# Optimization experiments

Measured on AMD Instinct MI355X. Metric: run time of the kernel, lower is better.

## Reference

```python
import jax, jax.numpy as jnp
import numpy as np

H = 16       # num_attention_heads
HKV = 4      # num_key_value_heads
D = 128      # head_dim
CHUNK = 64   # input_chunk_size
RBS = 64     # retrieval_block_size


def setup_inputs() -> dict:
    key = jax.random.key(0)
    ks = jax.random.split(key, 9)
    B, S, HID = 1, 2048, 2048
    RLEN = 2048  # retrieval_block_num * RBS = (S // CHUNK) * RBS
    inv = 0.02
    return {
        "hidden_states": jax.random.normal(ks[0], (B, S, HID), jnp.float32),
        "cos": jax.random.uniform(ks[1], (B, S, D), jnp.float32),
        "sin": jax.random.uniform(ks[2], (B, S, D), jnp.float32),
        "retrieval_k": jax.random.normal(ks[3], (B, HKV, RLEN, D), jnp.float32),
        "retrieval_v": jax.random.normal(ks[4], (B, HKV, RLEN, D), jnp.float32),
        "Wq": jax.random.normal(ks[5], (HID, H * D), jnp.float32) * inv,
        "Wk": jax.random.normal(ks[6], (HID, HKV * D), jnp.float32) * inv,
        "Wv": jax.random.normal(ks[7], (HID, HKV * D), jnp.float32) * inv,
        "Wo": jax.random.normal(ks[8], (H * D, HID), jnp.float32) * inv,
    }


def _rope(x, cos, sin):
    # x: [B, h, S, D]; cos/sin: [B, S, D] (HF apply_rotary_pos_emb, unsqueeze head dim)
    c = cos[:, None, :, :]
    s = sin[:, None, :, :]
    x1, x2 = jnp.split(x, 2, axis=-1)
    rot = jnp.concatenate([-x2, x1], axis=-1)
    return x * c + rot * s


def reference(hidden_states, cos, sin, retrieval_k, retrieval_v, Wq, Wk, Wv, Wo):
    B, S, HID = hidden_states.shape
    G = H // HKV
    scale = D ** -0.5

    q = (hidden_states @ Wq).reshape(B, S, H, D).transpose(0, 2, 1, 3)    # [B,H,S,D]
    k = (hidden_states @ Wk).reshape(B, S, HKV, D).transpose(0, 2, 1, 3)  # [B,HKV,S,D]
    v = (hidden_states @ Wv).reshape(B, S, HKV, D).transpose(0, 2, 1, 3)

    q = _rope(q, cos, sin)
    k = _rope(k, cos, sin)

    # GQA: expand kv heads
    k_full = jnp.repeat(k, G, axis=1)  # [B,H,S,D]
    v_full = jnp.repeat(v, G, axis=1)

    # ---- causal part over input keys ----
    s1 = jnp.einsum('bhqd,bhkd->bhqk', q, k_full) * scale
    causal = jnp.tril(jnp.ones((S, S), bool))
    s1 = jnp.where(causal[None, None], s1, -jnp.inf)

    # ---- retrieval part: chunk c attends retrieval block (c-1) only ----
    C = S // CHUNK
    R = retrieval_k.shape[2] // RBS
    rK = retrieval_k.reshape(B, HKV, R, RBS, D)
    rV = retrieval_v.reshape(B, HKV, R, RBS, D)
    blk_idx = jnp.clip(jnp.arange(C) - 1, 0, R - 1)          # chunk 0 masked below
    rK_sel = jnp.repeat(rK[:, :, blk_idx], G, axis=1)        # [B,H,C,RBS,D]
    rV_sel = jnp.repeat(rV[:, :, blk_idx], G, axis=1)
    qc = q.reshape(B, H, C, CHUNK, D)
    s2 = jnp.einsum('bhcqd,bhckd->bhcqk', qc, rK_sel) * scale
    valid = (jnp.arange(C) >= 1)[None, None, :, None, None]
    s2 = jnp.where(valid, s2, -jnp.inf)

    # ---- joint (numerically stable) softmax over causal + retrieval keys ----
    m1 = jnp.max(s1, axis=-1)                                # [B,H,S]
    m2 = jnp.max(s2, axis=-1).reshape(B, H, S)               # -inf for chunk 0
    m = jnp.maximum(m1, m2)
    e1 = jnp.exp(s1 - m[..., None])
    e2 = jnp.exp(s2 - m.reshape(B, H, C, CHUNK)[..., None])
    denom = e1.sum(-1) + e2.sum(-1).reshape(B, H, S)         # [B,H,S]
    o1 = jnp.einsum('bhqk,bhkd->bhqd', e1, v_full)
    o2 = jnp.einsum('bhcqk,bhckd->bhcqd', e2, rV_sel).reshape(B, H, S, D)
    attn = (o1 + o2) / denom[..., None]                      # [B,H,S,D]

    out = attn.transpose(0, 2, 1, 3).reshape(B, S, H * D)
    return out @ Wo
```

## Files before the change

### kernel.cpp

```cpp
#include <hip/hip_runtime.h>
#include <stdint.h>

#define H_    16
#define HKV_  4
#define D_    128
#define S_    2048
#define HID_  2048
#define RLEN_ 2048

typedef unsigned short u16;
typedef __attribute__((ext_vector_type(4))) float f32x4;
typedef __attribute__((ext_vector_type(16))) float f32x16;
typedef __attribute__((ext_vector_type(8))) __bf16 bf16x8;
typedef __attribute__((ext_vector_type(4))) unsigned short u16x4;
typedef __attribute__((ext_vector_type(8))) unsigned short u16x8;
typedef __attribute__((ext_vector_type(2))) unsigned int u32x2;

__device__ __forceinline__ u16 f2bf(float f) {
  union { float f; unsigned u; } v; v.f = f;
  unsigned r = v.u + 0x7FFFu + ((v.u >> 16) & 1u);
  return (u16)(r >> 16);
}
__device__ __forceinline__ float bf2f(u16 h) {
  union { unsigned u; float f; } v; v.u = ((unsigned)h) << 16;
  return v.f;
}
__device__ __forceinline__ float lo2f(unsigned w) {
  union { unsigned u; float f; } v; v.u = w << 16; return v.f;
}
__device__ __forceinline__ float hi2f(unsigned w) {
  union { unsigned u; float f; } v; v.u = w & 0xFFFF0000u; return v.f;
}
__device__ __forceinline__ float exp2v(float x) {
  float r; asm("v_exp_f32 %0, %1" : "=v"(r) : "v"(x)); return r;
}
__device__ __forceinline__ unsigned cvtpk(float lo, float hi) {
  unsigned r; asm("v_cvt_pk_bf16_f32 %0, %1, %2" : "=v"(r) : "v"(lo), "v"(hi)); return r;
}
__device__ __forceinline__ void pl32swap(unsigned &a, unsigned &b) {
  u32x2 r = __builtin_amdgcn_permlane32_swap(a, b, false, false);
  a = r.x; b = r.y;
}
__device__ __forceinline__ float xhalf_max(float v) {
  unsigned a = __float_as_uint(v), b = a;
  pl32swap(a, b);
  return fmaxf(__uint_as_float(a), __uint_as_float(b));
}
__device__ __forceinline__ float xhalf_add(float v) {
  unsigned a = __float_as_uint(v), b = a;
  pl32swap(a, b);
  return __uint_as_float(a) + __uint_as_float(b);
}
__device__ __forceinline__ void drain_then_sync() {
  asm volatile("s_waitcnt vmcnt(0) lgkmcnt(0)" ::: "memory");
  __syncthreads();
}

#define GLL(srcp, ldsp) \
  __builtin_amdgcn_global_load_lds((const __attribute__((address_space(1))) unsigned int*)(srcp), \
                                   (__attribute__((address_space(3))) unsigned int*)(ldsp), 16, 0, 0)

__global__ void k_cvt(const float* __restrict__ in, u16* __restrict__ out, int n4) {
  int i = blockIdx.x * 256 + threadIdx.x;
  if (i >= n4) return;
  float4 v = ((const float4*)in)[i];
  u16x4 o;
  o.x = f2bf(v.x); o.y = f2bf(v.y); o.z = f2bf(v.z); o.w = f2bf(v.w);
  ((u16x4*)out)[i] = o;
}

__global__ void k_transw_qkv(const float* __restrict__ Wq, const float* __restrict__ Wk,
                             const float* __restrict__ Wv, u16* __restrict__ wtq) {
  __shared__ float tile[32][33];
  const int bid = blockIdx.x;
  const float* in; u16* out; int N, bx, by;
  if (bid < 4096)      { in = Wq; out = wtq;                          N = 2048; bx = (bid & 63) * 32;        by = (bid >> 6) * 32; }
  else if (bid < 5120) { in = Wk; out = wtq + (size_t)2048 * 2048;    N = 512;  bx = ((bid - 4096) & 15) * 32; by = ((bid - 4096) >> 4) * 32; }
  else                 { in = Wv; out = wtq + (size_t)2560 * 2048;    N = 512;  bx = ((bid - 5120) & 15) * 32; by = ((bid - 5120) >> 4) * 32; }
  const int K = 2048;
  int tx = threadIdx.x, ty = threadIdx.y;
#pragma unroll
  for (int i = 0; i < 32; i += 8)
    tile[ty + i][tx] = in[(size_t)(by + ty + i) * N + bx + tx];
  __syncthreads();
#pragma unroll
  for (int i = 0; i < 32; i += 8)
    out[(size_t)(bx + ty + i) * K + by + tx] = f2bf(tile[tx][ty + i]);
}

__global__ void k_transw(const float* __restrict__ in, u16* __restrict__ out, int K, int N) {
  __shared__ float tile[32][33];
  int bx = blockIdx.x * 32, by = blockIdx.y * 32;
  int tx = threadIdx.x, ty = threadIdx.y;
#pragma unroll
  for (int i = 0; i < 32; i += 8)
    tile[ty + i][tx] = in[(size_t)(by + ty + i) * N + bx + tx];
  __syncthreads();
#pragma unroll
  for (int i = 0; i < 32; i += 8)
    out[(size_t)(bx + ty + i) * K + by + tx] = f2bf(tile[tx][ty + i]);
}

__global__ __launch_bounds__(256) void k_gemm(const u16* __restrict__ A, const u16* __restrict__ Bt,
                                              u16* __restrict__ Cb, int M, int N, int K,
                                              int Kpart, int Krem) {
  __shared__ __attribute__((aligned(16))) u16 As[2][128 * 32];
  __shared__ __attribute__((aligned(16))) u16 Bs[2][128 * 32];
  const int bm = blockIdx.y * 128, bn = blockIdx.x * 128;
  const int kz0 = blockIdx.z * Kpart;
  const int kz1 = kz0 + Kpart + ((blockIdx.z == gridDim.z - 1) ? Krem : 0);
  u16* C = Cb + (size_t)blockIdx.z * M * N;
  const int tid = threadIdx.x, wave = tid >> 6, lane = tid & 63;
  const int wr = wave >> 1, wc = wave & 1;
  const int l15 = lane & 15, lhi = lane >> 4;
  const int so = wave * 512;
  f32x4 acc[4][4] = {};
  const u16* pA  = A  + (size_t)(bm + (tid >> 2)) * K + (tid & 3) * 8;
  const u16* pA2 = A  + (size_t)(bm + 64 + (tid >> 2)) * K + (tid & 3) * 8;
  const u16* pB  = Bt + (size_t)(bn + (tid >> 2)) * K + (tid & 3) * 8;
  const u16* pB2 = Bt + (size_t)(bn + 64 + (tid >> 2)) * K + (tid & 3) * 8;

  GLL(pA + kz0,  &As[0][so]);
  GLL(pA2 + kz0, &As[0][2048 + so]);
  GLL(pB + kz0,  &Bs[0][so]);
  GLL(pB2 + kz0, &Bs[0][2048 + so]);
  drain_then_sync();

  int buf = 0;
  for (int k0 = kz0; k0 < kz1; k0 += 32) {
    const int nb = buf ^ 1;
    if (k0 + 32 < kz1) {
      GLL(pA + k0 + 32,  &As[nb][so]);
      GLL(pA2 + k0 + 32, &As[nb][2048 + so]);
      GLL(pB + k0 + 32,  &Bs[nb][so]);
      GLL(pB2 + k0 + 32, &Bs[nb][2048 + so]);
    }
    bf16x8 af[4], bfr[4];
#pragma unroll
    for (int m = 0; m < 4; m++)
      af[m] = *(const bf16x8*)(&As[buf][(wr * 64 + m * 16 + l15) * 32 + lhi * 8]);
#pragma unroll
    for (int n = 0; n < 4; n++)
      bfr[n] = *(const bf16x8*)(&Bs[buf][(wc * 64 + n * 16 + l15) * 32 + lhi * 8]);
#pragma unroll
    for (int m = 0; m < 4; m++)
#pragma unroll
      for (int n = 0; n < 4; n++)
        acc[m][n] = __builtin_amdgcn_mfma_f32_16x16x32_bf16(af[m], bfr[n], acc[m][n], 0, 0, 0);
    drain_then_sync();
    buf = nb;
  }
  const int r0 = bm + wr * 64, c0 = bn + wc * 64;
#pragma unroll
  for (int m = 0; m < 4; m++)
#pragma unroll
    for (int n = 0; n < 4; n++) {
      int r = r0 + m * 16 + lhi * 4, cc = c0 + n * 16 + l15;
#pragma unroll
      for (int j = 0; j < 4; j++)
        C[(size_t)(r + j) * N + cc] = f2bf(acc[m][n][j]);
    }
}

__global__ void k_comb2(const u16* __restrict__ c0, const u16* __restrict__ c1,
                        float* __restrict__ out, int n8) {
  int i = blockIdx.x * 256 + threadIdx.x;
  if (i >= n8) return;
  u16x8 a = ((const u16x8*)c0)[i];
  u16x8 b = ((const u16x8*)c1)[i];
  float4 o0, o1;
  o0.x = bf2f(a[0]) + bf2f(b[0]); o0.y = bf2f(a[1]) + bf2f(b[1]);
  o0.z = bf2f(a[2]) + bf2f(b[2]); o0.w = bf2f(a[3]) + bf2f(b[3]);
  o1.x = bf2f(a[4]) + bf2f(b[4]); o1.y = bf2f(a[5]) + bf2f(b[5]);
  o1.z = bf2f(a[6]) + bf2f(b[6]); o1.w = bf2f(a[7]) + bf2f(b[7]);
  ((float4*)out)[i * 2]     = o0;
  ((float4*)out)[i * 2 + 1] = o1;
}

__global__ void k_ropeq(const u16* __restrict__ qp0, const float* __restrict__ cs,
                        const float* __restrict__ sn, u16* __restrict__ Q) {
  const u16* qp1 = qp0 + (size_t)2048 * 3072;
  int tid = threadIdx.x;
  int idx = blockIdx.x * 4 + (tid >> 6);
  int d = tid & 63;
  int h = idx >> 11, s = idx & (S_ - 1);
  size_t base = (size_t)s * 3072 + h * 128;
  float x1 = bf2f(qp0[base + d])      + bf2f(qp1[base + d]);
  float x2 = bf2f(qp0[base + d + 64]) + bf2f(qp1[base + d + 64]);
  float c1 = cs[s * D_ + d], s1v = sn[s * D_ + d];
  float c2 = cs[s * D_ + d + 64], s2v = sn[s * D_ + d + 64];
  const float sc = 0.12751744422f;
  u16* o = Q + ((size_t)h * S_ + s) * D_;
  o[d]      = f2bf((x1 * c1 - x2 * s1v) * sc);
  o[d + 64] = f2bf((x2 * c2 + x1 * s2v) * sc);
}

__global__ void k_ropekv(const u16* __restrict__ qp0, const float* __restrict__ cs,
                         const float* __restrict__ sn, u16* __restrict__ Ksw,
                         u16* __restrict__ Vts) {
  const u16* qp1 = qp0 + (size_t)2048 * 3072;
  int tid = threadIdx.x;
  int idx = blockIdx.x * 4 + (tid >> 6);
  int d = tid & 63;
  int kv = idx >> 11, s = idx & (S_ - 1);
  size_t kb = (size_t)s * 3072 + 2048 + kv * 128;
  size_t vb = kb + 512;
  float x1 = bf2f(qp0[kb + d])      + bf2f(qp1[kb + d]);
  float x2 = bf2f(qp0[kb + d + 64]) + bf2f(qp1[kb + d + 64]);
  float v1 = bf2f(qp0[vb + d])      + bf2f(qp1[vb + d]);
  float v2 = bf2f(qp0[vb + d + 64]) + bf2f(qp1[vb + d + 64]);
  float c1 = cs[s * D_ + d], s1v = sn[s * D_ + d];
  float c2 = cs[s * D_ + d + 64], s2v = sn[s * D_ + d + 64];
  u16* ko = Ksw + ((size_t)kv * S_ + s) * D_;
  int sw = (s & 7) << 3;
  ko[d ^ sw]        = f2bf(x1 * c1 - x2 * s1v);
  ko[(d + 64) ^ sw] = f2bf(x2 * c2 + x1 * s2v);
  u16* vo = Vts + (size_t)kv * D_ * S_;
  int sc64 = s & ~63, sl = s & 63;
  vo[(size_t)d * S_        + sc64 + (sl ^ ((d & 7) << 3))]        = f2bf(v1);
  vo[(size_t)(d + 64) * S_ + sc64 + (sl ^ (((d + 64) & 7) << 3))] = f2bf(v2);
}

__global__ void k_retr(const float* __restrict__ rk, const float* __restrict__ rv,
                       u16* __restrict__ Krs, u16* __restrict__ Vtrs) {
  int tid = threadIdx.x;
  int idx = blockIdx.x * 2 + (tid >> 7);
  int d = tid & 127;
  int kv = idx >> 11, r = idx & (RLEN_ - 1);
  size_t base = ((size_t)kv * RLEN_ + r) * D_;
  Krs[base + (d ^ ((r & 7) << 3))] = f2bf(rk[base + d]);
  int rc = r & ~63, rl = r & 63;
  Vtrs[((size_t)kv * D_ + d) * RLEN_ + rc + (rl ^ ((d & 7) << 3))] = f2bf(rv[base + d]);
}

__global__ __launch_bounds__(256, 3) void k_attn(
    const u16* __restrict__ Q, const u16* __restrict__ Ksw, const u16* __restrict__ Vts,
    const u16* __restrict__ Krs, const u16* __restrict__ Vtrs,
    u16* __restrict__ Opart, float* __restrict__ Ml) {
  __shared__ __attribute__((aligned(16))) char smem[32768];
  u16* Kl = (u16*)smem;
  u16* Vl = (u16*)(smem + 16384);

  const int e = 83 - blockIdx.x, h = blockIdx.y, kvh = h >> 2;
  int c, part, np;
  if (e < 7)       { c = e;               part = 0;           np = 1; }
  else if (e < 23) { c = 7 + ((e - 7) >> 1);  part = (e - 7) & 1;  np = 2; }
  else if (e < 47) { c = 15 + (e - 23) / 3;   part = (e - 23) % 3; np = 3; }
  else if (e < 79) { c = 23 + ((e - 47) >> 2); part = (e - 47) & 3; np = 4; }
  else             { c = 31;              part = e - 79;      np = 5; }
  const int nt = (c == 0) ? 1 : (c + 2);
  const int t0 = (part * nt) / np, t1 = ((part + 1) * nt) / np;
  const int bp = h * 84 + e;

  const int tid = threadIdx.x, wave = tid >> 6, lane = tid & 63;
  const int qs = wave & 1, kp = wave >> 1;
  const int l31 = lane & 31, hf = lane >> 5;
  const int qrow = c * 64 + qs * 32 + l31;

  bf16x8 qf[8];
  {
    const u16* qp = Q + ((size_t)h * S_ + qrow) * D_ + hf * 8;
#pragma unroll
    for (int m = 0; m < 8; m++) qf[m] = *(const bf16x8*)(qp + m * 16);
  }
  float mq = -1e30f, lq = 0.f;
  f32x16 accO[4] = {};

  const int kgo = (tid >> 4) * 128 + (tid & 15) * 8;
  const int vgo = (tid >> 3) * 2048 + (tid & 7) * 8;
  u16* const kdst = Kl + wave * 512;
  u16* const vdst = Vl + wave * 512;

  const int cm1 = (c >= 1) ? (c - 1) : 0;
  const u16* krb = Krs + (size_t)kvh * RLEN_ * D_ + (size_t)cm1 * 64 * D_;
  const u16* vrb = Vtrs + (size_t)kvh * D_ * RLEN_ + cm1 * 64;
  const u16* kst = Ksw + (size_t)kvh * S_ * D_ + (size_t)t0 * 64 * D_;
  const u16* vst = Vts + (size_t)kvh * D_ * S_ + t0 * 64;
  int ts = t0;

#pragma unroll
  for (int p = 0; p < 4; p++) GLL(kst + p * 2048 + kgo, kdst + p * 2048);
#pragma unroll
  for (int p = 0; p < 4; p++) GLL(vst + p * 65536 + vgo, vdst + p * 2048);
  ts = t0 + 1;
  if (ts == c + 1) { kst = krb; vst = vrb; } else { kst += 64 * D_; vst += 64; }
  drain_then_sync();

  for (int t = t0; t < t1; t++) {
    const bool pf = (t + 1 < t1);
    f32x16 sacc = {};
    {
      const char* Kbuf = (const char*)Kl;
#pragma unroll
      for (int m = 0; m < 8; m++) {
        int by = ((kp * 32 + l31) << 8) + ((m * 32 + hf * 16) ^ ((l31 & 7) << 4));
        bf16x8 kf = *(const bf16x8*)(Kbuf + by);
        sacc = __builtin_amdgcn_mfma_f32_32x32x16_bf16(kf, qf[m], sacc, 0, 0, 0);
      }
    }
    drain_then_sync();
    if (pf) {
#pragma unroll
      for (int p = 0; p < 4; p++) GLL(kst + p * 2048 + kgo, kdst + p * 2048);
    }
    if (t == c) {
      const int koffm = (kp - qs) * 32;
#pragma unroll
      for (int r = 0; r < 16; r++) {
        int kloc = (r & 3) + 8 * (r >> 2) + 4 * hf + koffm;
        if (kloc > l31) sacc[r] = -1e30f;
      }
    }
    float tmax = sacc[0];
#pragma unroll
    for (int r = 1; r < 16; r++) tmax = fmaxf(tmax, sacc[r]);
    tmax = xhalf_max(tmax);
    if (!__all(tmax - mq <= 11.5f)) {
      float mn = fmaxf(mq, tmax);
      float f = exp2v(mq - mn);
      mq = mn; lq *= f;
#pragma unroll
      for (int dt = 0; dt < 4; dt++)
#pragma unroll
        for (int r = 0; r < 16; r++) accO[dt][r] *= f;
    }
    float ps = 0.f;
#pragma unroll
    for (int r = 0; r < 16; r++) {
      float p = exp2v(sacc[r] - mq);
      sacc[r] = p; ps += p;
    }
    lq += xhalf_add(ps);
    unsigned W[8];
#pragma unroll
    for (int g = 0; g < 4; g++) {
      W[2 * g]     = cvtpk(sacc[4 * g],     sacc[4 * g + 1]);
      W[2 * g + 1] = cvtpk(sacc[4 * g + 2], sacc[4 * g + 3]);
    }
    const char* Vbuf = (const char*)Vl;
    __builtin_amdgcn_s_setprio(1);
#pragma unroll
    for (int st = 0; st < 2; st++) {
      unsigned x0 = W[4 * st], y0 = W[4 * st + 2];
      unsigned x1 = W[4 * st + 1], y1 = W[4 * st + 3];
      pl32swap(x0, y0);
      pl32swap(x1, y1);
      union { unsigned u[4]; bf16x8 v; } pfr;
      pfr.u[0] = x0; pfr.u[1] = x1; pfr.u[2] = y0; pfr.u[3] = y1;
#pragma unroll
      for (int dt = 0; dt < 4; dt++) {
        int vby = ((dt * 32 + l31) << 7) + ((kp * 64 + st * 32 + hf * 16) ^ ((l31 & 7) << 4));
        bf16x8 vf = *(const bf16x8*)(Vbuf + vby);
        accO[dt] = __builtin_amdgcn_mfma_f32_32x32x16_bf16(vf, pfr.v, accO[dt], 0, 0, 0);
      }
    }
    __builtin_amdgcn_s_setprio(0);
    drain_then_sync();
    if (pf) {
#pragma unroll
      for (int p = 0; p < 4; p++) GLL(vst + p * 65536 + vgo, vdst + p * 2048);
      ts++;
      if (ts == c + 1) { kst = krb; vst = vrb; } else { kst += 64 * D_; vst += 64; }
    }
  }

  unsigned* mrg = (unsigned*)smem;
  const int mbase = (qs * 64 + lane) * 36;
  if (kp == 1) {
#pragma unroll
    for (int dt = 0; dt < 4; dt++)
#pragma unroll
      for (int k2 = 0; k2 < 8; k2++)
        mrg[mbase + dt * 8 + k2] = cvtpk(accO[dt][2 * k2], accO[dt][2 * k2 + 1]);
    mrg[mbase + 32] = __float_as_uint(mq);
    mrg[mbase + 33] = __float_as_uint(lq);
  }
  drain_then_sync();
  if (kp == 0) {
    float m1 = __uint_as_float(mrg[mbase + 32]);
    float l1 = __uint_as_float(mrg[mbase + 33]);
    float mm = fmaxf(mq, m1);
    float w0 = exp2v(mq - mm), w1 = exp2v(m1 - mm);
    float ll = w0 * lq + w1 * l1;
    u16* op = Opart + (size_t)bp * 8192 + (size_t)(qs * 32 + l31) * 128;
#pragma unroll
    for (int dt = 0; dt < 4; dt++)
#pragma unroll
      for (int j = 0; j < 4; j++) {
        u16x4 o;
#pragma unroll
        for (int b = 0; b < 4; b++) {
          int r = 4 * j + b;
          unsigned pw = mrg[mbase + dt * 8 + (r >> 1)];
          float pv = (r & 1) ? hi2f(pw) : lo2f(pw);
          o[b] = f2bf(w0 * accO[dt][r] + w1 * pv);
        }
        *(u16x4*)(op + dt * 32 + j * 8 + hf * 4) = o;
      }
    if (hf == 0) {
      Ml[(size_t)bp * 128 + qs * 32 + l31]      = mm;
      Ml[(size_t)bp * 128 + 64 + qs * 32 + l31] = ll;
    }
  }
}

__global__ __launch_bounds__(256) void k_combine(const u16* __restrict__ Opart,
                                                 const float* __restrict__ Ml,
                                                 u16* __restrict__ attn) {
  const int c = blockIdx.x, h = blockIdx.y;
  const int t = threadIdx.x;
  const int q = t >> 2, d0 = (t & 3) * 32;
  int base, np;
  if (c < 7)       { base = c;                 np = 1; }
  else if (c < 15) { base = 7 + 2 * (c - 7);   np = 2; }
  else if (c < 23) { base = 23 + 3 * (c - 15); np = 3; }
  else if (c < 31) { base = 47 + 4 * (c - 23); np = 4; }
  else             { base = 79;                np = 5; }
  const size_t pb = (size_t)h * 84 + base;

  float m = -1e30f;
  for (int p = 0; p < np; p++) m = fmaxf(m, Ml[(pb + p) * 128 + q]);
  float l = 0.f;
  float N[32];
#pragma unroll
  for (int i = 0; i < 32; i++) N[i] = 0.f;
  for (int p = 0; p < np; p++) {
    const float mp = Ml[(pb + p) * 128 + q];
    const float lp = Ml[(pb + p) * 128 + 64 + q];
    const float w = exp2v(mp - m);
    l += w * lp;
    const u16* op = Opart + (pb + p) * 8192 + q * 128 + d0;
#pragma unroll
    for (int i = 0; i < 4; i++) {
      u16x8 v = ((const u16x8*)op)[i];
#pragma unroll
      for (int ee = 0; ee < 8; ee++) N[i * 8 + ee] += w * bf2f(v[ee]);
    }
  }
  const float inv = 1.f / l;
  u16* dst = attn + (size_t)(c * 64 + q) * (H_ * D_) + h * 128 + d0;
#pragma unroll
  for (int i = 0; i < 4; i++) {
    u16x8 o;
#pragma unroll
    for (int ee = 0; ee < 8; ee++) o[ee] = f2bf(N[i * 8 + ee] * inv);
    ((u16x8*)dst)[i] = o;
  }
}

extern "C" void kernel_launch(void* const* d_in, const int* in_sizes, int n_in,
                              void* d_out, int out_size, void* d_ws, size_t ws_size,
                              hipStream_t stream) {
  const float* hs = (const float*)d_in[0];
  const float* cs = (const float*)d_in[1];
  const float* sn = (const float*)d_in[2];
  const float* rk = (const float*)d_in[3];
  const float* rv = (const float*)d_in[4];
  const float* Wq = (const float*)d_in[5];
  const float* Wk = (const float*)d_in[6];
  const float* Wv = (const float*)d_in[7];
  const float* Wo = (const float*)d_in[8];
  float* out = (float*)d_out;
  char* ws = (char*)d_ws;
  if (ws_size < (size_t)(56u << 20)) return;

  u16* hsb  = (u16*)(ws);
  u16* wtq  = (u16*)(ws + (8u << 20));
  u16* qkvP = (u16*)(ws + (20u << 20));
  u16* Qr   = (u16*)(ws + (44u << 20));
  u16* Ks   = (u16*)(ws + (52u << 20));
  u16* Vts  = (u16*)(ws + (54u << 20));
  u16* Krs  = (u16*)(ws + (8u << 20));
  u16* Vtrs = (u16*)(ws + (10u << 20));
  u16* wto  = (u16*)(ws + (12u << 20));
  u16* Opart= (u16*)(ws + (20u << 20));
  float* Ml = (float*)(ws + (41u << 20));
  u16* attn = (u16*)(ws);
  u16* Cp   = (u16*)(ws + (20u << 20));

  dim3 tb(32, 8);
  k_cvt<<<4096, 256, 0, stream>>>(hs, hsb, 1048576);
  k_transw_qkv<<<6144, tb, 0, stream>>>(Wq, Wk, Wv, wtq);
  k_gemm<<<dim3(24, 16, 2), 256, 0, stream>>>(hsb, wtq, qkvP, 2048, 3072, 2048, 1024, 0);
  k_ropeq<<<8192, 256, 0, stream>>>(qkvP, cs, sn, Qr);
  k_ropekv<<<2048, 256, 0, stream>>>(qkvP, cs, sn, Ks, Vts);
  k_retr<<<4096, 256, 0, stream>>>(rk, rv, Krs, Vtrs);
  k_transw<<<dim3(64, 64), tb, 0, stream>>>(Wo, wto, 2048, 2048);
  k_attn<<<dim3(84, 16), 256, 0, stream>>>(Qr, Ks, Vts, Krs, Vtrs, Opart, Ml);
  k_combine<<<dim3(32, 16), 256, 0, stream>>>(Opart, Ml, attn);
  k_gemm<<<dim3(16, 16, 2), 256, 0, stream>>>(attn, wto, Cp, 2048, 2048, 2048, 1024, 0);
  k_comb2<<<2048, 256, 0, stream>>>(Cp, Cp + (size_t)2048 * 2048, out, 524288);
}
```

Baseline: 161.8 us.

## Share K/V tiles across GQA head group in attention workgroup

```diff
diff --git a/kernel.cpp b/kernel.cpp
--- a/kernel.cpp
+++ b/kernel.cpp
@@ -24,12 +24,6 @@
 __device__ __forceinline__ float bf2f(u16 h) {
   union { unsigned u; float f; } v; v.u = ((unsigned)h) << 16;
   return v.f;
-}
-__device__ __forceinline__ float lo2f(unsigned w) {
-  union { unsigned u; float f; } v; v.u = w << 16; return v.f;
-}
-__device__ __forceinline__ float hi2f(unsigned w) {
-  union { unsigned u; float f; } v; v.u = w & 0xFFFF0000u; return v.f;
 }
 __device__ __forceinline__ float exp2v(float x) {
   float r; asm("v_exp_f32 %0, %1" : "=v"(r) : "v"(x)); return r;
@@ -241,7 +235,7 @@
   u16* Kl = (u16*)smem;
   u16* Vl = (u16*)(smem + 16384);
 
-  const int e = 83 - blockIdx.x, h = blockIdx.y, kvh = h >> 2;
+  const int e = 83 - blockIdx.x, kvh = blockIdx.y, qs = blockIdx.z;
   int c, part, np;
   if (e < 7)       { c = e;               part = 0;           np = 1; }
   else if (e < 23) { c = 7 + ((e - 7) >> 1);  part = (e - 7) & 1;  np = 2; }
@@ -250,10 +244,10 @@
   else             { c = 31;              part = e - 79;      np = 5; }
   const int nt = (c == 0) ? 1 : (c + 2);
   const int t0 = (part * nt) / np, t1 = ((part + 1) * nt) / np;
+
+  const int tid = threadIdx.x, wave = tid >> 6, lane = tid & 63;
+  const int h = kvh * 4 + wave;
   const int bp = h * 84 + e;
-
-  const int tid = threadIdx.x, wave = tid >> 6, lane = tid & 63;
-  const int qs = wave & 1, kp = wave >> 1;
   const int l31 = lane & 31, hf = lane >> 5;
   const int qrow = c * 64 + qs * 32 + l31;
 
@@ -288,15 +282,17 @@
 
   for (int t = t0; t < t1; t++) {
     const bool pf = (t + 1 < t1);
-    f32x16 sacc = {};
+    f32x16 sacc[2] = {};
     {
       const char* Kbuf = (const char*)Kl;
 #pragma unroll
-      for (int m = 0; m < 8; m++) {
-        int by = ((kp * 32 + l31) << 8) + ((m * 32 + hf * 16) ^ ((l31 & 7) << 4));
-        bf16x8 kf = *(const bf16x8*)(Kbuf + by);
-        sacc = __builtin_amdgcn_mfma_f32_32x32x16_bf16(kf, qf[m], sacc, 0, 0, 0);
-      }
+      for (int kb = 0; kb < 2; kb++)
+#pragma unroll
+        for (int m = 0; m < 8; m++) {
+          int by = ((kb * 32 + l31) << 8) + ((m * 32 + hf * 16) ^ ((l31 & 7) << 4));
+          bf16x8 kf = *(const bf16x8*)(Kbuf + by);
+          sacc[kb] = __builtin_amdgcn_mfma_f32_32x32x16_bf16(kf, qf[m], sacc[kb], 0, 0, 0);
+        }
     }
     drain_then_sync();
     if (pf) {
@@ -304,16 +300,21 @@
       for (int p = 0; p < 4; p++) GLL(kst + p * 2048 + kgo, kdst + p * 2048);
     }
     if (t == c) {
-      const int koffm = (kp - qs) * 32;
-#pragma unroll
-      for (int r = 0; r < 16; r++) {
-        int kloc = (r & 3) + 8 * (r >> 2) + 4 * hf + koffm;
-        if (kloc > l31) sacc[r] = -1e30f;
+#pragma unroll
+      for (int kb = 0; kb < 2; kb++) {
+        const int koffm = kb * 32 - qs * 32;
+#pragma unroll
+        for (int r = 0; r < 16; r++) {
+          int kloc = (r & 3) + 8 * (r >> 2) + 4 * hf + koffm;
+          if (kloc > l31) sacc[kb][r] = -1e30f;
+        }
       }
     }
-    float tmax = sacc[0];
-#pragma unroll
-    for (int r = 1; r < 16; r++) tmax = fmaxf(tmax, sacc[r]);
+    float tmax = sacc[0][0];
+#pragma unroll
+    for (int r = 1; r < 16; r++) tmax = fmaxf(tmax, sacc[0][r]);
+#pragma unroll
+    for (int r = 0; r < 16; r++) tmax = fmaxf(tmax, sacc[1][r]);
     tmax = xhalf_max(tmax);
     if (!__all(tmax - mq <= 11.5f)) {
       float mn = fmaxf(mq, tmax);
@@ -326,34 +327,41 @@
     }
     float ps = 0.f;
 #pragma unroll
-    for (int r = 0; r < 16; r++) {
-      float p = exp2v(sacc[r] - mq);
-      sacc[r] = p; ps += p;
-    }
+    for (int kb = 0; kb < 2; kb++)
+#pragma unroll
+      for (int r = 0; r < 16; r++) {
+        float p = exp2v(sacc[kb][r] - mq);
+        sacc[kb][r] = p; ps += p;
+      }
     lq += xhalf_add(ps);
-    unsigned W[8];
-#pragma unroll
-    for (int g = 0; g < 4; g++) {
-      W[2 * g]     = cvtpk(sacc[4 * g],     sacc[4 * g + 1]);
-      W[2 * g + 1] = cvtpk(sacc[4 * g + 2], sacc[4 * g + 3]);
-    }
+    unsigned W[2][8];
+#pragma unroll
+    for (int kb = 0; kb < 2; kb++)
+#pragma unroll
+      for (int g = 0; g < 4; g++) {
+        W[kb][2 * g]     = cvtpk(sacc[kb][4 * g],     sacc[kb][4 * g + 1]);
+        W[kb][2 * g + 1] = cvtpk(sacc[kb][4 * g + 2], sacc[kb][4 * g + 3]);
+      }
     const char* Vbuf = (const char*)Vl;
     __builtin_amdgcn_s_setprio(1);
 #pragma unroll
-    for (int st = 0; st < 2; st++) {
-      unsigned x0 = W[4 * st], y0 = W[4 * st + 2];
-      unsigned x1 = W[4 * st + 1], y1 = W[4 * st + 3];
-      pl32swap(x0, y0);
-      pl32swap(x1, y1);
-      union { unsigned u[4]; bf16x8 v; } pfr;
-      pfr.u[0] = x0; pfr.u[1] = x1; pfr.u[2] = y0; pfr.u[3] = y1;
-#pragma unroll
-      for (int dt = 0; dt < 4; dt++) {
-        int vby = ((dt * 32 + l31) << 7) + ((kp * 64 + st * 32 + hf * 16) ^ ((l31 & 7) << 4));
-        bf16x8 vf = *(const bf16x8*)(Vbuf + vby);
-        accO[dt] = __builtin_amdgcn_mfma_f32_32x32x16_bf16(vf, pfr.v, accO[dt], 0, 0, 0);
+    for (int kb = 0; kb < 2; kb++)
+#pragma unroll
+      for (int st = 0; st < 2; st++) {
+        unsigned x0 = W[kb][4 * st], y0 = W[kb][4 * st + 2];
+        unsigned x1 = W[kb][4 * st + 1], y1 = W[kb][4 * st + 3];
+        pl32swap(x0, y0);
+        pl32swap(x1, y1);
+        union { unsigned u[4]; bf16x8 v; } pfr;
+        pfr.u[0] = x0; pfr.u[1] = x1; pfr.u[2] = y0; pfr.u[3] = y1;
+#pragma unroll
+        for (int dt = 0; dt < 4; dt++) {
+          int vby = ((dt * 32 + l31) << 7) +
+                    ((kb * 64 + st * 32 + hf * 16) ^ ((l31 & 7) << 4));
+          bf16x8 vf = *(const bf16x8*)(Vbuf + vby);
+          accO[dt] = __builtin_amdgcn_mfma_f32_32x32x16_bf16(vf, pfr.v, accO[dt], 0, 0, 0);
+        }
       }
-    }
     __builtin_amdgcn_s_setprio(0);
     drain_then_sync();
     if (pf) {
@@ -364,43 +372,19 @@
     }
   }
 
-  unsigned* mrg = (unsigned*)smem;
-  const int mbase = (qs * 64 + lane) * 36;
-  if (kp == 1) {
-#pragma unroll
-    for (int dt = 0; dt < 4; dt++)
-#pragma unroll
-      for (int k2 = 0; k2 < 8; k2++)
-        mrg[mbase + dt * 8 + k2] = cvtpk(accO[dt][2 * k2], accO[dt][2 * k2 + 1]);
-    mrg[mbase + 32] = __float_as_uint(mq);
-    mrg[mbase + 33] = __float_as_uint(lq);
-  }
-  drain_then_sync();
-  if (kp == 0) {
-    float m1 = __uint_as_float(mrg[mbase + 32]);
-    float l1 = __uint_as_float(mrg[mbase + 33]);
-    float mm = fmaxf(mq, m1);
-    float w0 = exp2v(mq - mm), w1 = exp2v(m1 - mm);
-    float ll = w0 * lq + w1 * l1;
-    u16* op = Opart + (size_t)bp * 8192 + (size_t)(qs * 32 + l31) * 128;
-#pragma unroll
-    for (int dt = 0; dt < 4; dt++)
-#pragma unroll
-      for (int j = 0; j < 4; j++) {
-        u16x4 o;
-#pragma unroll
-        for (int b = 0; b < 4; b++) {
-          int r = 4 * j + b;
-          unsigned pw = mrg[mbase + dt * 8 + (r >> 1)];
-          float pv = (r & 1) ? hi2f(pw) : lo2f(pw);
-          o[b] = f2bf(w0 * accO[dt][r] + w1 * pv);
-        }
-        *(u16x4*)(op + dt * 32 + j * 8 + hf * 4) = o;
-      }
-    if (hf == 0) {
-      Ml[(size_t)bp * 128 + qs * 32 + l31]      = mm;
-      Ml[(size_t)bp * 128 + 64 + qs * 32 + l31] = ll;
-    }
+  u16* op = Opart + (size_t)bp * 8192 + (size_t)(qs * 32 + l31) * 128;
+#pragma unroll
+  for (int dt = 0; dt < 4; dt++)
+#pragma unroll
+    for (int j = 0; j < 4; j++) {
+      u16x4 o;
+#pragma unroll
+      for (int b = 0; b < 4; b++) o[b] = f2bf(accO[dt][4 * j + b]);
+      *(u16x4*)(op + dt * 32 + j * 8 + hf * 4) = o;
+    }
+  if (hf == 0) {
+    Ml[(size_t)bp * 128 + qs * 32 + l31]      = mq;
+    Ml[(size_t)bp * 128 + 64 + qs * 32 + l31] = lq;
   }
 }
 
@@ -486,7 +470,7 @@
   k_ropekv<<<2048, 256, 0, stream>>>(qkvP, cs, sn, Ks, Vts);
   k_retr<<<4096, 256, 0, stream>>>(rk, rv, Krs, Vtrs);
   k_transw<<<dim3(64, 64), tb, 0, stream>>>(Wo, wto, 2048, 2048);
-  k_attn<<<dim3(84, 16), 256, 0, stream>>>(Qr, Ks, Vts, Krs, Vtrs, Opart, Ml);
+  k_attn<<<dim3(84, 4, 2), 256, 0, stream>>>(Qr, Ks, Vts, Krs, Vtrs, Opart, Ml);
   k_combine<<<dim3(32, 16), 256, 0, stream>>>(Opart, Ml, attn);
   k_gemm<<<dim3(16, 16, 2), 256, 0, stream>>>(attn, wto, Cp, 2048, 2048, 2048, 1024, 0);
   k_comb2<<<2048, 256, 0, stream>>>(Cp, Cp + (size_t)2048 * 2048, out, 524288);
```

After: 160.0 us. Within noise of the previous version (-1.1%).
